# Performance work log

Measured on AMD Instinct MI355X. Metric: run time of the kernel, lower is better.

Reference implementation:

```python
import jax, jax.numpy as jnp
import numpy as np

NUM_SPARSE = 26
VOCAB = 100000
EMB = 64
B = 2048
DENSE = 13
NUM_FEA = NUM_SPARSE + 1  # 26 embeddings + bottom-MLP output


def _xavier(key, shape):
    fan_in, fan_out = shape[0], shape[1]
    lim = jnp.sqrt(6.0 / (fan_in + fan_out))
    return jax.random.uniform(key, shape, jnp.float32, -lim, lim)


def setup_inputs() -> dict:
    key = jax.random.key(0)
    ks = jax.random.split(key, 20)
    inp = {
        "dense": jax.random.normal(ks[0], (B, DENSE), jnp.float32),
        "cat_idx": jax.random.randint(ks[1], (B, NUM_SPARSE), 0, VOCAB, jnp.int32),
        # stacked EmbeddingBag tables (all same vocab -> one [26, V, 64] tensor)
        "tables": _xavier(ks[2], (VOCAB, EMB))[None] * jnp.ones((NUM_SPARSE, 1, 1), jnp.float32) * 0
                  + jax.random.normal(ks[3], (NUM_SPARSE, VOCAB, EMB), jnp.float32) * 0.01,
        # bottom MLP: 13 -> 512 -> 256 -> 64
        "bw0": _xavier(ks[4], (DENSE, 512)), "bb0": jnp.zeros((512,), jnp.float32),
        "bw1": _xavier(ks[5], (512, 256)),   "bb1": jnp.zeros((256,), jnp.float32),
        "bw2": _xavier(ks[6], (256, EMB)),   "bb2": jnp.zeros((EMB,), jnp.float32),
        # top MLP: 415 -> 1024 -> 512 -> 256 -> 1
        "tw0": _xavier(ks[7], (EMB + NUM_FEA * (NUM_FEA - 1) // 2, 1024)), "tb0": jnp.zeros((1024,), jnp.float32),
        "tw1": _xavier(ks[8], (1024, 512)),  "tb1": jnp.zeros((512,), jnp.float32),
        "tw2": _xavier(ks[9], (512, 256)),   "tb2": jnp.zeros((256,), jnp.float32),
        "tw3": _xavier(ks[10], (256, 1)),    "tb3": jnp.zeros((1,), jnp.float32),
    }
    return inp


def reference(dense, cat_idx, tables, bw0, bb0, bw1, bb1, bw2, bb2,
              tw0, tb0, tw1, tb1, tw2, tb2, tw3, tb3):
    # bottom MLP on dense features -> [B, EMB]
    h = jax.nn.relu(dense @ bw0 + bb0)
    h = jax.nn.relu(h @ bw1 + bb1)
    bot = jax.nn.relu(h @ bw2 + bb2)

    # EmbeddingBag (single index per bag, sum mode == plain gather): [B, 26, EMB]
    feat_ids = jnp.arange(NUM_SPARSE)[None, :]  # [1, 26]
    emb = tables[feat_ids, cat_idx]             # [B, 26, EMB]

    # dot interaction: batched Gram matrix then lower-triangular gather
    T = jnp.concatenate([bot[:, None, :], emb], axis=1)  # [B, 27, EMB]
    Z = jnp.einsum("bif,bjf->bij", T, T)                  # [B, 27, 27]
    li, lj = np.tril_indices(NUM_FEA, k=-1)               # 351 pairs
    Zflat = Z[:, li, lj]                                  # [B, 351]

    R = jnp.concatenate([bot, Zflat], axis=1)             # [B, 415]

    # top MLP
    r = jax.nn.relu(R @ tw0 + tb0)
    r = jax.nn.relu(r @ tw1 + tb1)
    r = jax.nn.relu(r @ tw2 + tb2)
    out = jax.nn.sigmoid(r @ tw3 + tb3)                   # [B, 1]
    return out
```

## Files before the change

### kernel.cpp

```cpp
#include <hip/hip_runtime.h>
#include <hip/hip_bf16.h>


#define BATCH 2048
#define VOCAB 100000
#define EMB 64
#define NSPARSE 26
#define NFEA 27
#define NPAIR 351
#define RLD 416

typedef __attribute__((ext_vector_type(8))) __bf16 bf16x8;
typedef __attribute__((ext_vector_type(4))) float f32x4;
typedef __hip_bfloat16 bf16;

#define GLOAD16(g, l)                                                          \
    __builtin_amdgcn_global_load_lds(                                          \
        (const __attribute__((address_space(1))) unsigned int*)(g),            \
        (__attribute__((address_space(3))) unsigned int*)(l), 16, 0, 0)

__global__ __launch_bounds__(256) void gemm_bf16(
    const bf16* __restrict__ A,
    const bf16* __restrict__ Wt,
    const float* __restrict__ bias,
    bf16* __restrict__ C,
    int M, int N, int K, int ldC)
{
    __shared__ __align__(16) bf16 As[64 * 32];
    __shared__ __align__(16) bf16 Bs[64 * 32];

    const int t   = threadIdx.x;
    const int nbn = N >> 6;
    const int bm  = blockIdx.x / nbn;
    const int bn  = blockIdx.x % nbn;
    const int row0 = bm << 6, n0 = bn << 6;

    const int wid  = t >> 6, lane = t & 63;
    const int wr   = wid >> 1, wc = wid & 1;
    const int lr   = lane & 15;
    const int q    = lane >> 4;

    const int srow = t >> 2, sslot = t & 3;
    const int sswz = sslot ^ ((srow >> 1) & 3);
    const char* gA = (const char*)(A  + (size_t)(row0 + srow) * K) + sswz * 16;
    const char* gB = (const char*)(Wt + (size_t)(n0   + srow) * K) + sswz * 16;
    char* lA = (char*)As + t * 16;
    char* lB = (char*)Bs + t * 16;

    f32x4 acc[2][2] = {};

    const int arow0 = wr * 32 + lr;
    const int brow0 = wc * 32 + lr;

    for (int k0 = 0; k0 < K; k0 += 32) {
        GLOAD16(gA + (size_t)k0 * 2, lA);
        GLOAD16(gB + (size_t)k0 * 2, lB);
        __syncthreads();

        bf16x8 af[2], bf[2];
#pragma unroll
        for (int m = 0; m < 2; ++m) {
            const int r = arow0 + 16 * m;
            af[m] = *(const bf16x8*)((const char*)As + r * 64 +
                                     ((q ^ ((r >> 1) & 3)) << 4));
        }
#pragma unroll
        for (int n = 0; n < 2; ++n) {
            const int r = brow0 + 16 * n;
            bf[n] = *(const bf16x8*)((const char*)Bs + r * 64 +
                                     ((q ^ ((r >> 1) & 3)) << 4));
        }
#pragma unroll
        for (int m = 0; m < 2; ++m)
#pragma unroll
            for (int n = 0; n < 2; ++n)
                acc[m][n] = __builtin_amdgcn_mfma_f32_16x16x32_bf16(
                    af[m], bf[n], acc[m][n], 0, 0, 0);
        __syncthreads();
    }

#pragma unroll
    for (int n = 0; n < 2; ++n) {
        const int col = n0 + wc * 32 + 16 * n + lr;
        const float bv = bias[col];
#pragma unroll
        for (int m = 0; m < 2; ++m) {
#pragma unroll
            for (int i = 0; i < 4; ++i) {
                const int row = row0 + wr * 32 + 16 * m + q * 4 + i;
                float v = acc[m][n][i] + bv;
                v = fmaxf(v, 0.f);
                C[(size_t)row * ldC + col] = __float2bfloat16(v);
            }
        }
    }
}

struct WConvArgs {
    const float* src[6];
    bf16*        dst[6];
    int K[6], N[6], Kp[6], t0[7];
};

__global__ __launch_bounds__(256) void wconv_kernel(WConvArgs a)
{
    __shared__ float Ts[32][33];
    int w = 0;
    while (w < 5 && (int)blockIdx.x >= a.t0[w + 1]) ++w;
    const int rel = blockIdx.x - a.t0[w];
    const int K = a.K[w], N = a.N[w], Kp = a.Kp[w];
    const int nbn = N >> 5;
    const int tk = rel / nbn, tn = rel % nbn;
    const int tx = threadIdx.x & 31, ty = threadIdx.x >> 5;

    const float* src = a.src[w];
    bf16* dst = a.dst[w];

#pragma unroll
    for (int rr = 0; rr < 4; ++rr) {
        const int k = tk * 32 + ty + rr * 8;
        const int n = tn * 32 + tx;
        Ts[ty + rr * 8][tx] = (k < K) ? src[(size_t)k * N + n] : 0.f;
    }
    __syncthreads();
#pragma unroll
    for (int rr = 0; rr < 4; ++rr) {
        const int n = tn * 32 + ty + rr * 8;
        const int kp = tk * 32 + tx;
        dst[(size_t)n * Kp + kp] = __float2bfloat16(Ts[tx][ty + rr * 8]);
    }
}

__global__ __launch_bounds__(256) void densepad_kernel(
    const float* __restrict__ dense, bf16* __restrict__ out)
{
    const int i = blockIdx.x * 256 + threadIdx.x;
    const int b = i >> 5, c = i & 31;
    out[i] = (c < 13) ? __float2bfloat16(dense[b * 13 + c]) : __float2bfloat16(0.f);
}

__global__ __launch_bounds__(256) void interact_kernel(
    const int* __restrict__ cat_idx, const float* __restrict__ tables,
    bf16* __restrict__ R)
{
    __shared__ float T[NFEA][EMB + 1];

    const int b    = blockIdx.x;
    const int t    = threadIdx.x;
    const int g    = t >> 6;
    const int lane = t & 63;
    bf16* Rrow = R + (size_t)b * RLD;

    for (int f = g; f < NFEA; f += 4) {
        if (f == 0) {
            T[0][lane] = __bfloat162float(Rrow[lane]);
        } else {
            const int j   = f - 1;
            const int idx = cat_idx[b * NSPARSE + j];
            T[f][lane] = tables[((size_t)j * VOCAB + idx) * EMB + lane];
        }
    }
    __syncthreads();

    if (t == 0) Rrow[415] = __float2bfloat16(0.f);

    for (int p = t; p < NPAIR; p += 256) {
        int i = (int)((1.0f + sqrtf(1.0f + 8.0f * (float)p)) * 0.5f);
        while (i * (i - 1) / 2 > p) --i;
        while ((i + 1) * i / 2 <= p) ++i;
        const int j = p - i * (i - 1) / 2;
        float s = 0.f;
#pragma unroll 16
        for (int k = 0; k < EMB; ++k) s += T[i][k] * T[j][k];
        Rrow[EMB + p] = __float2bfloat16(s);
    }
}

__global__ __launch_bounds__(256) void top3_kernel(
    const bf16* __restrict__ A, const float* __restrict__ w,
    const float* __restrict__ bias, float* __restrict__ out)
{
    const int gid  = blockIdx.x * 256 + threadIdx.x;
    const int row  = gid >> 6;
    const int lane = gid & 63;

    const bf16* arow = A + (size_t)row * 256;
    float s = 0.f;
#pragma unroll
    for (int k = lane; k < 256; k += 64)
        s += __bfloat162float(arow[k]) * w[k];
#pragma unroll
    for (int off = 32; off; off >>= 1) s += __shfl_down(s, off);
    if (lane == 0) out[row] = 1.f / (1.f + expf(-(s + bias[0])));
}

extern "C" void kernel_launch(void* const* d_in, const int* in_sizes, int n_in,
                              void* d_out, int out_size, void* d_ws, size_t ws_size,
                              hipStream_t stream)
{
    const float* dense   = (const float*)d_in[0];
    const int*   cat_idx = (const int*)  d_in[1];
    const float* tables  = (const float*)d_in[2];
    const float* bw0 = (const float*)d_in[3];
    const float* bb0 = (const float*)d_in[4];
    const float* bw1 = (const float*)d_in[5];
    const float* bb1 = (const float*)d_in[6];
    const float* bw2 = (const float*)d_in[7];
    const float* bb2 = (const float*)d_in[8];
    const float* tw0 = (const float*)d_in[9];
    const float* tb0 = (const float*)d_in[10];
    const float* tw1 = (const float*)d_in[11];
    const float* tb1 = (const float*)d_in[12];
    const float* tw2 = (const float*)d_in[13];
    const float* tb2 = (const float*)d_in[14];
    const float* tw3 = (const float*)d_in[15];
    const float* tb3 = (const float*)d_in[16];

    bf16* p = (bf16*)d_ws;
    bf16* dense_bf = p; p += (size_t)BATCH * 32;
    bf16* h0   = p; p += (size_t)BATCH * 512;
    bf16* h1   = p; p += (size_t)BATCH * 256;
    bf16* R    = p; p += (size_t)BATCH * RLD;
    bf16* r0   = p; p += (size_t)BATCH * 1024;
    bf16* r1   = p; p += (size_t)BATCH * 512;
    bf16* r2   = p; p += (size_t)BATCH * 256;
    bf16* bw0t = p; p += 512 * 32;
    bf16* bw1t = p; p += 256 * 512;
    bf16* bw2t = p; p += 64 * 256;
    bf16* tw0t = p; p += 1024 * RLD;
    bf16* tw1t = p; p += 512 * 1024;
    bf16* tw2t = p; p += 256 * 512;
    float* out = (float*)d_out;

    WConvArgs wa;
    wa.src[0] = bw0;  wa.dst[0] = bw0t; wa.K[0] = 13;   wa.N[0] = 512;  wa.Kp[0] = 32;
    wa.src[1] = bw1;  wa.dst[1] = bw1t; wa.K[1] = 512;  wa.N[1] = 256;  wa.Kp[1] = 512;
    wa.src[2] = bw2;  wa.dst[2] = bw2t; wa.K[2] = 256;  wa.N[2] = 64;   wa.Kp[2] = 256;
    wa.src[3] = tw0;  wa.dst[3] = tw0t; wa.K[3] = 415;  wa.N[3] = 1024; wa.Kp[3] = RLD;
    wa.src[4] = tw1;  wa.dst[4] = tw1t; wa.K[4] = 1024; wa.N[4] = 512;  wa.Kp[4] = 1024;
    wa.src[5] = tw2;  wa.dst[5] = tw2t; wa.K[5] = 512;  wa.N[5] = 256;  wa.Kp[5] = 512;
    int tiles = 0;
    for (int w = 0; w < 6; ++w) {
        wa.t0[w] = tiles;
        tiles += (wa.Kp[w] >> 5) * (wa.N[w] >> 5);
    }
    wa.t0[6] = tiles;

    wconv_kernel<<<tiles, 256, 0, stream>>>(wa);
    densepad_kernel<<<(BATCH * 32) / 256, 256, 0, stream>>>(dense, dense_bf);

    gemm_bf16<<<(BATCH / 64) * (512 / 64), 256, 0, stream>>>(
        dense_bf, bw0t, bb0, h0, BATCH, 512, 32, 512);
    gemm_bf16<<<(BATCH / 64) * (256 / 64), 256, 0, stream>>>(
        h0, bw1t, bb1, h1, BATCH, 256, 512, 256);
    gemm_bf16<<<(BATCH / 64) * (64 / 64), 256, 0, stream>>>(
        h1, bw2t, bb2, R, BATCH, 64, 256, RLD);

    interact_kernel<<<BATCH, 256, 0, stream>>>(cat_idx, tables, R);

    gemm_bf16<<<(BATCH / 64) * (1024 / 64), 256, 0, stream>>>(
        R, tw0t, tb0, r0, BATCH, 1024, RLD, 1024);
    gemm_bf16<<<(BATCH / 64) * (512 / 64), 256, 0, stream>>>(
        r0, tw1t, tb1, r1, BATCH, 512, 1024, 512);
    gemm_bf16<<<(BATCH / 64) * (256 / 64), 256, 0, stream>>>(
        r1, tw2t, tb2, r2, BATCH, 256, 512, 256);
    top3_kernel<<<BATCH / 4, 256, 0, stream>>>(r2, tw3, tb3, out);
}
```

Baseline: 72.73 us.

## Template GEMM on K-tile depth and fuse dense padding into first GEMM

The GEMM kernel becomes a template on K-tile depth (32 or 64) with a matching LDS swizzle. Most layers use BK=64, which halves the number of K iterations and barriers, and the interaction row stride is padded to 448 so it divides evenly by 64. The standalone densepad kernel is removed: the first GEMM reads fp32 dense features directly and converts them to bf16 into LDS, saving one launch and a workspace round trip. The cost is doubled LDS per block, which may lower occupancy, and extra zero padding in the first top GEMM.

Measured after the change: 67.74 us. 6.9% less time.

```diff
diff --git a/kernel.cpp b/kernel.cpp
--- a/kernel.cpp
+++ b/kernel.cpp
@@ -8,7 +8,7 @@
 #define NSPARSE 26
 #define NFEA 27
 #define NPAIR 351
-#define RLD 416
+#define RLD 448
 
 typedef __attribute__((ext_vector_type(8))) __bf16 bf16x8;
 typedef __attribute__((ext_vector_type(4))) float f32x4;
@@ -19,15 +19,21 @@
         (const __attribute__((address_space(1))) unsigned int*)(g),            \
         (__attribute__((address_space(3))) unsigned int*)(l), 16, 0, 0)
 
+template<int BK, bool DENSEPAD>
 __global__ __launch_bounds__(256) void gemm_bf16(
-    const bf16* __restrict__ A,
+    const void* __restrict__ Araw,
     const bf16* __restrict__ Wt,
     const float* __restrict__ bias,
     bf16* __restrict__ C,
     int M, int N, int K, int ldC)
 {
-    __shared__ __align__(16) bf16 As[64 * 32];
-    __shared__ __align__(16) bf16 Bs[64 * 32];
+    constexpr int ROWB   = BK * 2;
+    constexpr int SLOTS  = BK / 8;
+    constexpr int PASSES = BK / 32;
+    constexpr int RPP    = 256 / SLOTS;
+
+    __shared__ __align__(16) bf16 As[64 * BK];
+    __shared__ __align__(16) bf16 Bs[64 * BK];
 
     const int t   = threadIdx.x;
     const int nbn = N >> 6;
@@ -40,44 +46,70 @@
     const int lr   = lane & 15;
     const int q    = lane >> 4;
 
-    const int srow = t >> 2, sslot = t & 3;
-    const int sswz = sslot ^ ((srow >> 1) & 3);
-    const char* gA = (const char*)(A  + (size_t)(row0 + srow) * K) + sswz * 16;
-    const char* gB = (const char*)(Wt + (size_t)(n0   + srow) * K) + sswz * 16;
-    char* lA = (char*)As + t * 16;
-    char* lB = (char*)Bs + t * 16;
+#define SWZ(row, s) ((BK == 64) ? ((s) ^ ((row) & 7)) : ((s) ^ (((row) >> 1) & 3)))
+
+    const int srow  = t / SLOTS;
+    const int sslot = t % SLOTS;
+
+    const bf16* Ab[PASSES];
+    const bf16* Bb[PASSES];
+#pragma unroll
+    for (int p = 0; p < PASSES; ++p) {
+        const int r = p * RPP + srow;
+        const int g = SWZ(r, sslot);
+        if (!DENSEPAD)
+            Ab[p] = (const bf16*)Araw + (size_t)(row0 + r) * K + g * 8;
+        Bb[p] = Wt + (size_t)(n0 + r) * K + g * 8;
+    }
 
     f32x4 acc[2][2] = {};
 
-    const int arow0 = wr * 32 + lr;
-    const int brow0 = wc * 32 + lr;
-
-    for (int k0 = 0; k0 < K; k0 += 32) {
-        GLOAD16(gA + (size_t)k0 * 2, lA);
-        GLOAD16(gB + (size_t)k0 * 2, lB);
+    for (int k0 = 0; k0 < K; k0 += BK) {
+        if (DENSEPAD) {
+            const float* Df = (const float*)Araw;
+#pragma unroll
+            for (int idx = t; idx < 64 * 32; idx += 256) {
+                const int r = idx >> 5, c = idx & 31;
+                const float v = (c < 13) ? Df[(size_t)(row0 + r) * 13 + c] : 0.f;
+                As[r * 32 + SWZ(r, c >> 3) * 8 + (c & 7)] = __float2bfloat16(v);
+            }
+        } else {
+#pragma unroll
+            for (int p = 0; p < PASSES; ++p)
+                GLOAD16(Ab[p] + k0, (char*)As + p * 4096 + t * 16);
+        }
+#pragma unroll
+        for (int p = 0; p < PASSES; ++p)
+            GLOAD16(Bb[p] + k0, (char*)Bs + p * 4096 + t * 16);
         __syncthreads();
 
-        bf16x8 af[2], bf[2];
-#pragma unroll
-        for (int m = 0; m < 2; ++m) {
-            const int r = arow0 + 16 * m;
-            af[m] = *(const bf16x8*)((const char*)As + r * 64 +
-                                     ((q ^ ((r >> 1) & 3)) << 4));
-        }
-#pragma unroll
-        for (int n = 0; n < 2; ++n) {
-            const int r = brow0 + 16 * n;
-            bf[n] = *(const bf16x8*)((const char*)Bs + r * 64 +
-                                     ((q ^ ((r >> 1) & 3)) << 4));
-        }
-#pragma unroll
-        for (int m = 0; m < 2; ++m)
-#pragma unroll
-            for (int n = 0; n < 2; ++n)
-                acc[m][n] = __builtin_amdgcn_mfma_f32_16x16x32_bf16(
-                    af[m], bf[n], acc[m][n], 0, 0, 0);
+        bf16x8 af[PASSES][2], bfr[PASSES][2];
+#pragma unroll
+        for (int kk = 0; kk < PASSES; ++kk) {
+#pragma unroll
+            for (int m = 0; m < 2; ++m) {
+                const int r = wr * 32 + 16 * m + lr;
+                af[kk][m] = *(const bf16x8*)((const char*)As + r * ROWB +
+                                             SWZ(r, kk * 4 + q) * 16);
+            }
+#pragma unroll
+            for (int n = 0; n < 2; ++n) {
+                const int r = wc * 32 + 16 * n + lr;
+                bfr[kk][n] = *(const bf16x8*)((const char*)Bs + r * ROWB +
+                                              SWZ(r, kk * 4 + q) * 16);
+            }
+        }
+#pragma unroll
+        for (int kk = 0; kk < PASSES; ++kk)
+#pragma unroll
+            for (int m = 0; m < 2; ++m)
+#pragma unroll
+                for (int n = 0; n < 2; ++n)
+                    acc[m][n] = __builtin_amdgcn_mfma_f32_16x16x32_bf16(
+                        af[kk][m], bfr[kk][n], acc[m][n], 0, 0, 0);
         __syncthreads();
     }
+#undef SWZ
 
 #pragma unroll
     for (int n = 0; n < 2; ++n) {
@@ -131,14 +163,6 @@
     }
 }
 
-__global__ __launch_bounds__(256) void densepad_kernel(
-    const float* __restrict__ dense, bf16* __restrict__ out)
-{
-    const int i = blockIdx.x * 256 + threadIdx.x;
-    const int b = i >> 5, c = i & 31;
-    out[i] = (c < 13) ? __float2bfloat16(dense[b * 13 + c]) : __float2bfloat16(0.f);
-}
-
 __global__ __launch_bounds__(256) void interact_kernel(
     const int* __restrict__ cat_idx, const float* __restrict__ tables,
     bf16* __restrict__ R)
@@ -162,7 +186,7 @@
     }
     __syncthreads();
 
-    if (t == 0) Rrow[415] = __float2bfloat16(0.f);
+    if (t < RLD - 415) Rrow[415 + t] = __float2bfloat16(0.f);
 
     for (int p = t; p < NPAIR; p += 256) {
         int i = (int)((1.0f + sqrtf(1.0f + 8.0f * (float)p)) * 0.5f);
@@ -217,7 +241,6 @@
     const float* tb3 = (const float*)d_in[16];
 
     bf16* p = (bf16*)d_ws;
-    bf16* dense_bf = p; p += (size_t)BATCH * 32;
     bf16* h0   = p; p += (size_t)BATCH * 512;
     bf16* h1   = p; p += (size_t)BATCH * 256;
     bf16* R    = p; p += (size_t)BATCH * RLD;
@@ -247,22 +270,21 @@
     wa.t0[6] = tiles;
 
     wconv_kernel<<<tiles, 256, 0, stream>>>(wa);
-    densepad_kernel<<<(BATCH * 32) / 256, 256, 0, stream>>>(dense, dense_bf);
-
-    gemm_bf16<<<(BATCH / 64) * (512 / 64), 256, 0, stream>>>(
-        dense_bf, bw0t, bb0, h0, BATCH, 512, 32, 512);
-    gemm_bf16<<<(BATCH / 64) * (256 / 64), 256, 0, stream>>>(
+
+    gemm_bf16<32, true ><<<(BATCH / 64) * (512 / 64), 256, 0, stream>>>(
+        dense, bw0t, bb0, h0, BATCH, 512, 32, 512);
+    gemm_bf16<64, false><<<(BATCH / 64) * (256 / 64), 256, 0, stream>>>(
         h0, bw1t, bb1, h1, BATCH, 256, 512, 256);
-    gemm_bf16<<<(BATCH / 64) * (64 / 64), 256, 0, stream>>>(
+    gemm_bf16<64, false><<<(BATCH / 64) * (64 / 64), 256, 0, stream>>>(
         h1, bw2t, bb2, R, BATCH, 64, 256, RLD);
 
     interact_kernel<<<BATCH, 256, 0, stream>>>(cat_idx, tables, R);
 
-    gemm_bf16<<<(BATCH / 64) * (1024 / 64), 256, 0, stream>>>(
+    gemm_bf16<64, false><<<(BATCH / 64) * (1024 / 64), 256, 0, stream>>>(
         R, tw0t, tb0, r0, BATCH, 1024, RLD, 1024);
-    gemm_bf16<<<(BATCH / 64) * (512 / 64), 256, 0, stream>>>(
+    gemm_bf16<64, false><<<(BATCH / 64) * (512 / 64), 256, 0, stream>>>(
         r0, tw1t, tb1, r1, BATCH, 512, 1024, 512);
-    gemm_bf16<<<(BATCH / 64) * (256 / 64), 256, 0, stream>>>(
+    gemm_bf16<64, false><<<(BATCH / 64) * (256 / 64), 256, 0, stream>>>(
         r1, tw2t, tb2, r2, BATCH, 256, 512, 256);
     top3_kernel<<<BATCH / 4, 256, 0, stream>>>(r2, tw3, tb3, out);
 }
```
